# Kernel tuning notes

Hardware: AMD Instinct MI355X
Metric: run time of the kernel (lower is better)

## Reference

```python
import jax, jax.numpy as jnp
import numpy as np
from math import sqrt

LOCAL_WINDOW = 32
STRIDE = 64


def _sparse_mask(L):
    # L_Q == L_K path of DozerAttention:
    #  - local window: diagonals at offsets 0..local_window//2 (both signs)
    #  - strided: diagonals at offsets 0, stride+1, 2*(stride+1), ... (both signs)
    i = jnp.arange(L)[:, None]
    j = jnp.arange(L)[None, :]
    d = jnp.abs(i - j)
    local = d <= (LOCAL_WINDOW // 2)
    strided = (d % (STRIDE + 1)) == 0
    return (local | strided).astype(jnp.float32)  # [L, L]


def setup_inputs() -> dict:
    key = jax.random.key(0)
    B, L, H, D = 2, 2048, 8, 64
    kq, kk, kv = jax.random.split(key, 3)
    queries = jax.random.normal(kq, (B, L, H, D), dtype=jnp.float32)
    keys = jax.random.normal(kk, (B, L, H, D), dtype=jnp.float32)
    values = jax.random.normal(kv, (B, L, H, D), dtype=jnp.float32)
    # TriangularCausalMask: True above the diagonal -> masked with -inf
    causal = jnp.triu(jnp.ones((L, L), dtype=bool), k=1)
    attn_mask = jnp.broadcast_to(causal[None, None], (B, 1, L, L))
    return {"queries": queries, "keys": keys, "values": values, "attn_mask": attn_mask}


def reference(queries, keys, values, attn_mask):
    B, L, H, D = queries.shape
    scale = 1.0 / sqrt(D)
    sm = _sparse_mask(L)  # [L, L]
    # Original fills a zero-initialized dense score tensor only at selected key
    # columns per query row; equivalent to dense QK^T elementwise-masked by sm
    # (non-selected entries stay exactly 0, NOT -inf -- faithful quirk).
    scores = jnp.einsum('blhe,bshe->bhls', queries, keys) * sm  # [B,H,L,L]
    scores = jnp.where(attn_mask, -jnp.inf, scores)
    A = jax.nn.softmax(scale * scores, axis=-1)  # dropout p=0.0 in this config
    V = jnp.einsum('bhls,bshd->blhd', A, values)  # [B,L,H,D]
    return V
```

## Files before the change

kernel.cpp:

```cpp
#include <hip/hip_runtime.h>

#define B_ 2
#define L_ 2048
#define H_ 8
#define D_ 64
#define W_ 16
#define SP_ 65
#define NC_ 128
#define NL2_ 8

__global__ void chunk_sums_k(const float* __restrict__ v, float* __restrict__ csum1) {
    int blk = blockIdx.x;
    int c  = blk % NC_;
    int bh = blk / NC_;
    int h = bh % H_;
    int b = bh / H_;
    int d = threadIdx.x;
    float s = 0.f;
    int l0 = c * 16;
    #pragma unroll
    for (int l = 0; l < 16; ++l)
        s += v[((b * L_ + l0 + l) * H_ + h) * D_ + d];
    csum1[(bh * NC_ + c) * D_ + d] = s;
}

__global__ void l2_sums_k(const float* __restrict__ csum1, float* __restrict__ csum2) {
    int blk = blockIdx.x;
    int c2 = blk % NL2_;
    int bh = blk / NL2_;
    int d  = threadIdx.x;
    float s = 0.f;
    #pragma unroll
    for (int cc = 0; cc < 16; ++cc)
        s += csum1[(bh * NC_ + c2 * 16 + cc) * D_ + d];
    csum2[(bh * NL2_ + c2) * D_ + d] = s;
}

__global__ __launch_bounds__(256) void dozer_k(const float* __restrict__ q,
                                               const float* __restrict__ k,
                                               const float* __restrict__ v,
                                               const float* __restrict__ csum1,
                                               const float* __restrict__ csum2,
                                               float* __restrict__ out) {
    int gtid = blockIdx.x * blockDim.x + threadIdx.x;
    int wave = gtid >> 6;
    int lane = threadIdx.x & 63;
    int grp  = lane >> 3;
    int sub  = lane & 7;
    int i  = wave % L_;
    int hh = (wave / L_) % H_;
    int b  = wave / (L_ * H_);
    int bh = b * H_ + hh;

    const int rowstride = H_ * D_;
    const float* qp = q + ((size_t)(b * L_ + i) * H_ + hh) * D_ + 8 * sub;
    float4 qa = *(const float4*)qp;
    float4 qb = *(const float4*)(qp + 4);

    const float* kbase = k + ((size_t)b * L_ * H_ + hh) * D_ + 8 * sub;
    const float* vbase = v + ((size_t)b * L_ * H_ + hh) * D_ + 8 * sub;

    float4 na = make_float4(0.f, 0.f, 0.f, 0.f);
    float4 nb = make_float4(0.f, 0.f, 0.f, 0.f);
    float z = 0.f;

    int c1 = i >> 4;
    int c2 = i >> 8;
    int pstart = c1 << 4;

    int omax = (i < W_) ? i : W_;
    for (int o = grp; o <= omax; o += 8) {
        int j = i - o;
        const float* kr = kbase + (size_t)j * rowstride;
        const float* vr = vbase + (size_t)j * rowstride;
        float4 ka = *(const float4*)kr;
        float4 kb = *(const float4*)(kr + 4);
        float4 va = *(const float4*)vr;
        float4 vb = *(const float4*)(vr + 4);
        float part = qa.x * ka.x + qa.y * ka.y + qa.z * ka.z + qa.w * ka.w
                   + qb.x * kb.x + qb.y * kb.y + qb.z * kb.z + qb.w * kb.w;
        part += __shfl_xor(part, 1, 64);
        part += __shfl_xor(part, 2, 64);
        part += __shfl_xor(part, 4, 64);
        float we = __expf(0.125f * part) - 1.f;
        z += we;
        float wv = we + ((j >= pstart) ? 1.f : 0.f);
        na.x += wv * va.x; na.y += wv * va.y; na.z += wv * va.z; na.w += wv * va.w;
        nb.x += wv * vb.x; nb.y += wv * vb.y; nb.z += wv * vb.z; nb.w += wv * vb.w;
    }

    int tmax = i / SP_;
    for (int t = 1 + grp; t <= tmax; t += 8) {
        int j = i - SP_ * t;
        const float* kr = kbase + (size_t)j * rowstride;
        const float* vr = vbase + (size_t)j * rowstride;
        float4 ka = *(const float4*)kr;
        float4 kb = *(const float4*)(kr + 4);
        float4 va = *(const float4*)vr;
        float4 vb = *(const float4*)(vr + 4);
        float part = qa.x * ka.x + qa.y * ka.y + qa.z * ka.z + qa.w * ka.w
                   + qb.x * kb.x + qb.y * kb.y + qb.z * kb.z + qb.w * kb.w;
        part += __shfl_xor(part, 1, 64);
        part += __shfl_xor(part, 2, 64);
        part += __shfl_xor(part, 4, 64);
        float we = __expf(0.125f * part) - 1.f;
        z += we;
        na.x += we * va.x; na.y += we * va.y; na.z += we * va.z; na.w += we * va.w;
        nb.x += we * vb.x; nb.y += we * vb.y; nb.z += we * vb.z; nb.w += we * vb.w;
    }

    const float* cs2 = csum2 + ((size_t)bh * NL2_) * D_ + 8 * sub;
    for (int cc = grp; cc < c2; cc += 8) {
        float4 a = *(const float4*)(cs2 + (size_t)cc * D_);
        float4 bb = *(const float4*)(cs2 + (size_t)cc * D_ + 4);
        na.x += a.x; na.y += a.y; na.z += a.z; na.w += a.w;
        nb.x += bb.x; nb.y += bb.y; nb.z += bb.z; nb.w += bb.w;
    }
    const float* cs1 = csum1 + ((size_t)bh * NC_) * D_ + 8 * sub;
    for (int cc = (c2 << 4) + grp; cc < c1; cc += 8) {
        float4 a = *(const float4*)(cs1 + (size_t)cc * D_);
        float4 bb = *(const float4*)(cs1 + (size_t)cc * D_ + 4);
        na.x += a.x; na.y += a.y; na.z += a.z; na.w += a.w;
        nb.x += bb.x; nb.y += bb.y; nb.z += bb.z; nb.w += bb.w;
    }

    #pragma unroll
    for (int m = 8; m <= 32; m <<= 1) {
        na.x += __shfl_xor(na.x, m, 64); na.y += __shfl_xor(na.y, m, 64);
        na.z += __shfl_xor(na.z, m, 64); na.w += __shfl_xor(na.w, m, 64);
        nb.x += __shfl_xor(nb.x, m, 64); nb.y += __shfl_xor(nb.y, m, 64);
        nb.z += __shfl_xor(nb.z, m, 64); nb.w += __shfl_xor(nb.w, m, 64);
        z    += __shfl_xor(z, m, 64);
    }

    if (lane < 8) {
        float inv = 1.f / (z + (float)(i + 1));
        float* op = out + ((size_t)(b * L_ + i) * H_ + hh) * D_ + 8 * sub;
        float4 oa = make_float4(na.x * inv, na.y * inv, na.z * inv, na.w * inv);
        float4 ob = make_float4(nb.x * inv, nb.y * inv, nb.z * inv, nb.w * inv);
        *(float4*)op = oa;
        *(float4*)(op + 4) = ob;
    }
}

extern "C" void kernel_launch(void* const* d_in, const int* in_sizes, int n_in,
                              void* d_out, int out_size, void* d_ws, size_t ws_size,
                              hipStream_t stream) {
    const float* q = (const float*)d_in[0];
    const float* k = (const float*)d_in[1];
    const float* v = (const float*)d_in[2];
    float* out = (float*)d_out;

    float* csum1 = (float*)d_ws;
    float* csum2 = csum1 + (size_t)B_ * H_ * NC_ * D_;

    chunk_sums_k<<<B_ * H_ * NC_, 64, 0, stream>>>(v, csum1);
    l2_sums_k   <<<B_ * H_ * NL2_, 64, 0, stream>>>(csum1, csum2);

    int rows = B_ * H_ * L_;
    dozer_k<<<rows / 4, 256, 0, stream>>>(q, k, v, csum1, csum2, out);
}
```

Measured before the change: 124.5 us.

## Process two adjacent query rows per wave to share local-window K/V loads

Each wave now handles a pair of adjacent query rows (ia, ib). The local window loads 18 keys once and uses them for both rows, with predicates selecting which offsets count for each. The prefix chunk sums are also computed once and added to both rows, while the strided keys are still loaded separately per row. This halves the wave count and removes some redundant K/V and chunk-sum traffic, at the cost of more registers per thread and extra predication.

New measurement: 123.1 us. Within noise of the previous version (-1.1%).

```diff
diff --git a/kernel.cpp b/kernel.cpp
--- a/kernel.cpp
+++ b/kernel.cpp
@@ -47,99 +47,141 @@
     int lane = threadIdx.x & 63;
     int grp  = lane >> 3;
     int sub  = lane & 7;
-    int i  = wave % L_;
-    int hh = (wave / L_) % H_;
-    int b  = wave / (L_ * H_);
+    int pr = wave % (L_ / 2);
+    int hh = (wave / (L_ / 2)) % H_;
+    int b  = wave / ((L_ / 2) * H_);
     int bh = b * H_ + hh;
-
-    const int rowstride = H_ * D_;
-    const float* qp = q + ((size_t)(b * L_ + i) * H_ + hh) * D_ + 8 * sub;
-    float4 qa = *(const float4*)qp;
-    float4 qb = *(const float4*)(qp + 4);
+    int ia = 2 * pr;
+    int ib = ia + 1;
+
+    const int rs = H_ * D_;
+    const float* qpa = q + ((size_t)(b * L_ + ia) * H_ + hh) * D_ + 8 * sub;
+    float4 qa0 = *(const float4*)qpa;
+    float4 qa1 = *(const float4*)(qpa + 4);
+    float4 qb0 = *(const float4*)(qpa + rs);
+    float4 qb1 = *(const float4*)(qpa + rs + 4);
 
     const float* kbase = k + ((size_t)b * L_ * H_ + hh) * D_ + 8 * sub;
     const float* vbase = v + ((size_t)b * L_ * H_ + hh) * D_ + 8 * sub;
 
-    float4 na = make_float4(0.f, 0.f, 0.f, 0.f);
-    float4 nb = make_float4(0.f, 0.f, 0.f, 0.f);
-    float z = 0.f;
-
-    int c1 = i >> 4;
-    int c2 = i >> 8;
+    float4 na0 = make_float4(0.f,0.f,0.f,0.f), na1 = na0;
+    float4 nb0 = na0, nb1 = na0;
+    float za = 0.f, zb = 0.f;
+
+    int c1 = ia >> 4;
+    int c2 = ia >> 8;
     int pstart = c1 << 4;
 
-    int omax = (i < W_) ? i : W_;
-    for (int o = grp; o <= omax; o += 8) {
-        int j = i - o;
-        const float* kr = kbase + (size_t)j * rowstride;
-        const float* vr = vbase + (size_t)j * rowstride;
-        float4 ka = *(const float4*)kr;
-        float4 kb = *(const float4*)(kr + 4);
-        float4 va = *(const float4*)vr;
-        float4 vb = *(const float4*)(vr + 4);
-        float part = qa.x * ka.x + qa.y * ka.y + qa.z * ka.z + qa.w * ka.w
-                   + qb.x * kb.x + qb.y * kb.y + qb.z * kb.z + qb.w * kb.w;
-        part += __shfl_xor(part, 1, 64);
-        part += __shfl_xor(part, 2, 64);
-        part += __shfl_xor(part, 4, 64);
-        float we = __expf(0.125f * part) - 1.f;
-        z += we;
-        float wv = we + ((j >= pstart) ? 1.f : 0.f);
-        na.x += wv * va.x; na.y += wv * va.y; na.z += wv * va.z; na.w += wv * va.w;
-        nb.x += wv * vb.x; nb.y += wv * vb.y; nb.z += wv * vb.z; nb.w += wv * vb.w;
-    }
-
-    int tmax = i / SP_;
+    #pragma unroll
+    for (int it = 0; it < 3; ++it) {
+        int o = grp + 8 * it;
+        int j = ib - o;
+        bool jok = (o <= 17) && (j >= 0);
+        int jc = jok ? j : 0;
+        const float* kr = kbase + (size_t)jc * rs;
+        const float* vr = vbase + (size_t)jc * rs;
+        float4 k0 = *(const float4*)kr;
+        float4 k1 = *(const float4*)(kr + 4);
+        float4 v0 = *(const float4*)vr;
+        float4 v1 = *(const float4*)(vr + 4);
+        float pa = qa0.x*k0.x + qa0.y*k0.y + qa0.z*k0.z + qa0.w*k0.w
+                 + qa1.x*k1.x + qa1.y*k1.y + qa1.z*k1.z + qa1.w*k1.w;
+        float pb = qb0.x*k0.x + qb0.y*k0.y + qb0.z*k0.z + qb0.w*k0.w
+                 + qb1.x*k1.x + qb1.y*k1.y + qb1.z*k1.z + qb1.w*k1.w;
+        pa += __shfl_xor(pa, 1, 64); pb += __shfl_xor(pb, 1, 64);
+        pa += __shfl_xor(pa, 2, 64); pb += __shfl_xor(pb, 2, 64);
+        pa += __shfl_xor(pa, 4, 64); pb += __shfl_xor(pb, 4, 64);
+        bool act_a = jok && (o >= 1);
+        bool act_b = jok && (o <= 16);
+        float wa = act_a ? (__expf(0.125f * pa) - 1.f) : 0.f;
+        float wb = act_b ? (__expf(0.125f * pb) - 1.f) : 0.f;
+        za += wa; zb += wb;
+        float fa = wa + ((jok && o >= 1 && j >= pstart) ? 1.f : 0.f);
+        float fb = wb + ((jok && j >= pstart) ? 1.f : 0.f);
+        na0.x += fa*v0.x; na0.y += fa*v0.y; na0.z += fa*v0.z; na0.w += fa*v0.w;
+        na1.x += fa*v1.x; na1.y += fa*v1.y; na1.z += fa*v1.z; na1.w += fa*v1.w;
+        nb0.x += fb*v0.x; nb0.y += fb*v0.y; nb0.z += fb*v0.z; nb0.w += fb*v0.w;
+        nb1.x += fb*v1.x; nb1.y += fb*v1.y; nb1.z += fb*v1.z; nb1.w += fb*v1.w;
+    }
+
+    int tmax = ib / SP_;
     for (int t = 1 + grp; t <= tmax; t += 8) {
-        int j = i - SP_ * t;
-        const float* kr = kbase + (size_t)j * rowstride;
-        const float* vr = vbase + (size_t)j * rowstride;
-        float4 ka = *(const float4*)kr;
-        float4 kb = *(const float4*)(kr + 4);
-        float4 va = *(const float4*)vr;
-        float4 vb = *(const float4*)(vr + 4);
-        float part = qa.x * ka.x + qa.y * ka.y + qa.z * ka.z + qa.w * ka.w
-                   + qb.x * kb.x + qb.y * kb.y + qb.z * kb.z + qb.w * kb.w;
-        part += __shfl_xor(part, 1, 64);
-        part += __shfl_xor(part, 2, 64);
-        part += __shfl_xor(part, 4, 64);
-        float we = __expf(0.125f * part) - 1.f;
-        z += we;
-        na.x += we * va.x; na.y += we * va.y; na.z += we * va.z; na.w += we * va.w;
-        nb.x += we * vb.x; nb.y += we * vb.y; nb.z += we * vb.z; nb.w += we * vb.w;
-    }
-
-    const float* cs2 = csum2 + ((size_t)bh * NL2_) * D_ + 8 * sub;
+        int jb = ib - SP_ * t;
+        int ja = jb - 1;
+        bool aok = (ja >= 0);
+        int jac = aok ? ja : 0;
+        const float* kra = kbase + (size_t)jac * rs;
+        const float* vra = vbase + (size_t)jac * rs;
+        const float* krb = kbase + (size_t)jb * rs;
+        const float* vrb = vbase + (size_t)jb * rs;
+        float4 ka0 = *(const float4*)kra;
+        float4 ka1 = *(const float4*)(kra + 4);
+        float4 kb0 = *(const float4*)krb;
+        float4 kb1 = *(const float4*)(krb + 4);
+        float4 va0 = *(const float4*)vra;
+        float4 va1 = *(const float4*)(vra + 4);
+        float4 vb0 = *(const float4*)vrb;
+        float4 vb1 = *(const float4*)(vrb + 4);
+        float pa = qa0.x*ka0.x + qa0.y*ka0.y + qa0.z*ka0.z + qa0.w*ka0.w
+                 + qa1.x*ka1.x + qa1.y*ka1.y + qa1.z*ka1.z + qa1.w*ka1.w;
+        float pb = qb0.x*kb0.x + qb0.y*kb0.y + qb0.z*kb0.z + qb0.w*kb0.w
+                 + qb1.x*kb1.x + qb1.y*kb1.y + qb1.z*kb1.z + qb1.w*kb1.w;
+        pa += __shfl_xor(pa, 1, 64); pb += __shfl_xor(pb, 1, 64);
+        pa += __shfl_xor(pa, 2, 64); pb += __shfl_xor(pb, 2, 64);
+        pa += __shfl_xor(pa, 4, 64); pb += __shfl_xor(pb, 4, 64);
+        float wa = aok ? (__expf(0.125f * pa) - 1.f) : 0.f;
+        float wb = __expf(0.125f * pb) - 1.f;
+        za += wa; zb += wb;
+        na0.x += wa*va0.x; na0.y += wa*va0.y; na0.z += wa*va0.z; na0.w += wa*va0.w;
+        na1.x += wa*va1.x; na1.y += wa*va1.y; na1.z += wa*va1.z; na1.w += wa*va1.w;
+        nb0.x += wb*vb0.x; nb0.y += wb*vb0.y; nb0.z += wb*vb0.z; nb0.w += wb*vb0.w;
+        nb1.x += wb*vb1.x; nb1.y += wb*vb1.y; nb1.z += wb*vb1.z; nb1.w += wb*vb1.w;
+    }
+
+    float4 p0 = make_float4(0.f,0.f,0.f,0.f), p1 = p0;
+    const float* cs2 = csum2 + (size_t)bh * NL2_ * D_ + 8 * sub;
     for (int cc = grp; cc < c2; cc += 8) {
         float4 a = *(const float4*)(cs2 + (size_t)cc * D_);
-        float4 bb = *(const float4*)(cs2 + (size_t)cc * D_ + 4);
-        na.x += a.x; na.y += a.y; na.z += a.z; na.w += a.w;
-        nb.x += bb.x; nb.y += bb.y; nb.z += bb.z; nb.w += bb.w;
-    }
-    const float* cs1 = csum1 + ((size_t)bh * NC_) * D_ + 8 * sub;
+        float4 bq = *(const float4*)(cs2 + (size_t)cc * D_ + 4);
+        p0.x += a.x;  p0.y += a.y;  p0.z += a.z;  p0.w += a.w;
+        p1.x += bq.x; p1.y += bq.y; p1.z += bq.z; p1.w += bq.w;
+    }
+    const float* cs1 = csum1 + (size_t)bh * NC_ * D_ + 8 * sub;
     for (int cc = (c2 << 4) + grp; cc < c1; cc += 8) {
         float4 a = *(const float4*)(cs1 + (size_t)cc * D_);
-        float4 bb = *(const float4*)(cs1 + (size_t)cc * D_ + 4);
-        na.x += a.x; na.y += a.y; na.z += a.z; na.w += a.w;
-        nb.x += bb.x; nb.y += bb.y; nb.z += bb.z; nb.w += bb.w;
-    }
+        float4 bq = *(const float4*)(cs1 + (size_t)cc * D_ + 4);
+        p0.x += a.x;  p0.y += a.y;  p0.z += a.z;  p0.w += a.w;
+        p1.x += bq.x; p1.y += bq.y; p1.z += bq.z; p1.w += bq.w;
+    }
+    na0.x += p0.x; na0.y += p0.y; na0.z += p0.z; na0.w += p0.w;
+    na1.x += p1.x; na1.y += p1.y; na1.z += p1.z; na1.w += p1.w;
+    nb0.x += p0.x; nb0.y += p0.y; nb0.z += p0.z; nb0.w += p0.w;
+    nb1.x += p1.x; nb1.y += p1.y; nb1.z += p1.z; nb1.w += p1.w;
 
     #pragma unroll
     for (int m = 8; m <= 32; m <<= 1) {
-        na.x += __shfl_xor(na.x, m, 64); na.y += __shfl_xor(na.y, m, 64);
-        na.z += __shfl_xor(na.z, m, 64); na.w += __shfl_xor(na.w, m, 64);
-        nb.x += __shfl_xor(nb.x, m, 64); nb.y += __shfl_xor(nb.y, m, 64);
-        nb.z += __shfl_xor(nb.z, m, 64); nb.w += __shfl_xor(nb.w, m, 64);
-        z    += __shfl_xor(z, m, 64);
-    }
-
-    if (lane < 8) {
-        float inv = 1.f / (z + (float)(i + 1));
-        float* op = out + ((size_t)(b * L_ + i) * H_ + hh) * D_ + 8 * sub;
-        float4 oa = make_float4(na.x * inv, na.y * inv, na.z * inv, na.w * inv);
-        float4 ob = make_float4(nb.x * inv, nb.y * inv, nb.z * inv, nb.w * inv);
-        *(float4*)op = oa;
-        *(float4*)(op + 4) = ob;
+        na0.x += __shfl_xor(na0.x, m, 64); na0.y += __shfl_xor(na0.y, m, 64);
+        na0.z += __shfl_xor(na0.z, m, 64); na0.w += __shfl_xor(na0.w, m, 64);
+        na1.x += __shfl_xor(na1.x, m, 64); na1.y += __shfl_xor(na1.y, m, 64);
+        na1.z += __shfl_xor(na1.z, m, 64); na1.w += __shfl_xor(na1.w, m, 64);
+        nb0.x += __shfl_xor(nb0.x, m, 64); nb0.y += __shfl_xor(nb0.y, m, 64);
+        nb0.z += __shfl_xor(nb0.z, m, 64); nb0.w += __shfl_xor(nb0.w, m, 64);
+        nb1.x += __shfl_xor(nb1.x, m, 64); nb1.y += __shfl_xor(nb1.y, m, 64);
+        nb1.z += __shfl_xor(nb1.z, m, 64); nb1.w += __shfl_xor(nb1.w, m, 64);
+        za    += __shfl_xor(za, m, 64);
+        zb    += __shfl_xor(zb, m, 64);
+    }
+
+    if (grp == 0) {
+        float inv = 1.f / (za + (float)(ia + 1));
+        float* op = out + ((size_t)(b * L_ + ia) * H_ + hh) * D_ + 8 * sub;
+        *(float4*)op       = make_float4(na0.x*inv, na0.y*inv, na0.z*inv, na0.w*inv);
+        *(float4*)(op + 4) = make_float4(na1.x*inv, na1.y*inv, na1.z*inv, na1.w*inv);
+    } else if (grp == 1) {
+        float inv = 1.f / (zb + (float)(ib + 1));
+        float* op = out + ((size_t)(b * L_ + ib) * H_ + hh) * D_ + 8 * sub;
+        *(float4*)op       = make_float4(nb0.x*inv, nb0.y*inv, nb0.z*inv, nb0.w*inv);
+        *(float4*)(op + 4) = make_float4(nb1.x*inv, nb1.y*inv, nb1.z*inv, nb1.w*inv);
     }
 }
 
@@ -157,6 +199,6 @@
     chunk_sums_k<<<B_ * H_ * NC_, 64, 0, stream>>>(v, csum1);
     l2_sums_k   <<<B_ * H_ * NL2_, 64, 0, stream>>>(csum1, csum2);
 
-    int rows = B_ * H_ * L_;
-    dozer_k<<<rows / 4, 256, 0, stream>>>(q, k, v, csum1, csum2, out);
-}
+    int pairs = B_ * H_ * (L_ / 2);
+    dozer_k<<<pairs / 4, 256, 0, stream>>>(q, k, v, csum1, csum2, out);
+}
```

## Split each query row across two waves and combine partial sums in LDS

Applied to the files above, without the earlier changes.

Each query row is now handled by two waves, 16 key slots per row instead of 8, with the partial numerators and normalizers combined through shared memory after a block barrier. The grid doubles to compensate. The aim is to shorten the per-wave serial loop over the local, strided and prefix-sum terms, which cuts per-row latency and gives more parallelism. In exchange it adds a __syncthreads and LDS traffic, and duplicates the q load and setup work across both waves.

New measurement: 130.8 us. +5.1%, slower.

```diff
diff --git a/kernel.cpp b/kernel.cpp
--- a/kernel.cpp
+++ b/kernel.cpp
@@ -42,26 +42,31 @@
                                                const float* __restrict__ csum1,
                                                const float* __restrict__ csum2,
                                                float* __restrict__ out) {
-    int gtid = blockIdx.x * blockDim.x + threadIdx.x;
-    int wave = gtid >> 6;
+    __shared__ float sm[4][72];
+    __shared__ float zs[4];
+
     int lane = threadIdx.x & 63;
+    int wib  = threadIdx.x >> 6;
     int grp  = lane >> 3;
     int sub  = lane & 7;
-    int i  = wave % L_;
-    int hh = (wave / L_) % H_;
-    int b  = wave / (L_ * H_);
-    int bh = b * H_ + hh;
+    int half = wib & 1;
+    int slot = grp + 8 * half;
 
-    const int rowstride = H_ * D_;
+    int R  = 2 * blockIdx.x + (wib >> 1);
+    int i  = R & (L_ - 1);
+    int bh = R >> 11;
+    int hh = bh & (H_ - 1);
+    int b  = bh >> 3;
+
+    const int rs = H_ * D_;
     const float* qp = q + ((size_t)(b * L_ + i) * H_ + hh) * D_ + 8 * sub;
-    float4 qa = *(const float4*)qp;
-    float4 qb = *(const float4*)(qp + 4);
+    float4 q0 = *(const float4*)qp;
+    float4 q1 = *(const float4*)(qp + 4);
 
     const float* kbase = k + ((size_t)b * L_ * H_ + hh) * D_ + 8 * sub;
     const float* vbase = v + ((size_t)b * L_ * H_ + hh) * D_ + 8 * sub;
 
-    float4 na = make_float4(0.f, 0.f, 0.f, 0.f);
-    float4 nb = make_float4(0.f, 0.f, 0.f, 0.f);
+    float4 n0 = make_float4(0.f, 0.f, 0.f, 0.f), n1 = n0;
     float z = 0.f;
 
     int c1 = i >> 4;
@@ -69,77 +74,81 @@
     int pstart = c1 << 4;
 
     int omax = (i < W_) ? i : W_;
-    for (int o = grp; o <= omax; o += 8) {
+    for (int o = slot; o <= omax; o += 16) {
         int j = i - o;
-        const float* kr = kbase + (size_t)j * rowstride;
-        const float* vr = vbase + (size_t)j * rowstride;
-        float4 ka = *(const float4*)kr;
-        float4 kb = *(const float4*)(kr + 4);
-        float4 va = *(const float4*)vr;
-        float4 vb = *(const float4*)(vr + 4);
-        float part = qa.x * ka.x + qa.y * ka.y + qa.z * ka.z + qa.w * ka.w
-                   + qb.x * kb.x + qb.y * kb.y + qb.z * kb.z + qb.w * kb.w;
-        part += __shfl_xor(part, 1, 64);
-        part += __shfl_xor(part, 2, 64);
-        part += __shfl_xor(part, 4, 64);
-        float we = __expf(0.125f * part) - 1.f;
+        const float* kr = kbase + (size_t)j * rs;
+        const float* vr = vbase + (size_t)j * rs;
+        float4 k0 = *(const float4*)kr;
+        float4 k1 = *(const float4*)(kr + 4);
+        float4 v0 = *(const float4*)vr;
+        float4 v1 = *(const float4*)(vr + 4);
+        float p = q0.x*k0.x + q0.y*k0.y + q0.z*k0.z + q0.w*k0.w
+                + q1.x*k1.x + q1.y*k1.y + q1.z*k1.z + q1.w*k1.w;
+        p += __shfl_xor(p, 1, 64);
+        p += __shfl_xor(p, 2, 64);
+        p += __shfl_xor(p, 4, 64);
+        float we = __expf(0.125f * p) - 1.f;
         z += we;
         float wv = we + ((j >= pstart) ? 1.f : 0.f);
-        na.x += wv * va.x; na.y += wv * va.y; na.z += wv * va.z; na.w += wv * va.w;
-        nb.x += wv * vb.x; nb.y += wv * vb.y; nb.z += wv * vb.z; nb.w += wv * vb.w;
+        n0.x += wv*v0.x; n0.y += wv*v0.y; n0.z += wv*v0.z; n0.w += wv*v0.w;
+        n1.x += wv*v1.x; n1.y += wv*v1.y; n1.z += wv*v1.z; n1.w += wv*v1.w;
     }
 
     int tmax = i / SP_;
-    for (int t = 1 + grp; t <= tmax; t += 8) {
+    for (int t = 1 + slot; t <= tmax; t += 16) {
         int j = i - SP_ * t;
-        const float* kr = kbase + (size_t)j * rowstride;
-        const float* vr = vbase + (size_t)j * rowstride;
-        float4 ka = *(const float4*)kr;
-        float4 kb = *(const float4*)(kr + 4);
-        float4 va = *(const float4*)vr;
-        float4 vb = *(const float4*)(vr + 4);
-        float part = qa.x * ka.x + qa.y * ka.y + qa.z * ka.z + qa.w * ka.w
-                   + qb.x * kb.x + qb.y * kb.y + qb.z * kb.z + qb.w * kb.w;
-        part += __shfl_xor(part, 1, 64);
-        part += __shfl_xor(part, 2, 64);
-        part += __shfl_xor(part, 4, 64);
-        float we = __expf(0.125f * part) - 1.f;
+        const float* kr = kbase + (size_t)j * rs;
+        const float* vr = vbase + (size_t)j * rs;
+        float4 k0 = *(const float4*)kr;
+        float4 k1 = *(const float4*)(kr + 4);
+        float4 v0 = *(const float4*)vr;
+        float4 v1 = *(const float4*)(vr + 4);
+        float p = q0.x*k0.x + q0.y*k0.y + q0.z*k0.z + q0.w*k0.w
+                + q1.x*k1.x + q1.y*k1.y + q1.z*k1.z + q1.w*k1.w;
+        p += __shfl_xor(p, 1, 64);
+        p += __shfl_xor(p, 2, 64);
+        p += __shfl_xor(p, 4, 64);
+        float we = __expf(0.125f * p) - 1.f;
         z += we;
-        na.x += we * va.x; na.y += we * va.y; na.z += we * va.z; na.w += we * va.w;
-        nb.x += we * vb.x; nb.y += we * vb.y; nb.z += we * vb.z; nb.w += we * vb.w;
+        n0.x += we*v0.x; n0.y += we*v0.y; n0.z += we*v0.z; n0.w += we*v0.w;
+        n1.x += we*v1.x; n1.y += we*v1.y; n1.z += we*v1.z; n1.w += we*v1.w;
     }
 
-    const float* cs2 = csum2 + ((size_t)bh * NL2_) * D_ + 8 * sub;
-    for (int cc = grp; cc < c2; cc += 8) {
+    const float* cs2 = csum2 + (size_t)bh * NL2_ * D_ + 8 * sub;
+    for (int cc = slot; cc < c2; cc += 16) {
         float4 a = *(const float4*)(cs2 + (size_t)cc * D_);
         float4 bb = *(const float4*)(cs2 + (size_t)cc * D_ + 4);
-        na.x += a.x; na.y += a.y; na.z += a.z; na.w += a.w;
-        nb.x += bb.x; nb.y += bb.y; nb.z += bb.z; nb.w += bb.w;
+        n0.x += a.x;  n0.y += a.y;  n0.z += a.z;  n0.w += a.w;
+        n1.x += bb.x; n1.y += bb.y; n1.z += bb.z; n1.w += bb.w;
     }
-    const float* cs1 = csum1 + ((size_t)bh * NC_) * D_ + 8 * sub;
-    for (int cc = (c2 << 4) + grp; cc < c1; cc += 8) {
+    const float* cs1 = csum1 + (size_t)bh * NC_ * D_ + 8 * sub;
+    for (int cc = (c2 << 4) + slot; cc < c1; cc += 16) {
         float4 a = *(const float4*)(cs1 + (size_t)cc * D_);
         float4 bb = *(const float4*)(cs1 + (size_t)cc * D_ + 4);
-        na.x += a.x; na.y += a.y; na.z += a.z; na.w += a.w;
-        nb.x += bb.x; nb.y += bb.y; nb.z += bb.z; nb.w += bb.w;
+        n0.x += a.x;  n0.y += a.y;  n0.z += a.z;  n0.w += a.w;
+        n1.x += bb.x; n1.y += bb.y; n1.z += bb.z; n1.w += bb.w;
     }
 
     #pragma unroll
     for (int m = 8; m <= 32; m <<= 1) {
-        na.x += __shfl_xor(na.x, m, 64); na.y += __shfl_xor(na.y, m, 64);
-        na.z += __shfl_xor(na.z, m, 64); na.w += __shfl_xor(na.w, m, 64);
-        nb.x += __shfl_xor(nb.x, m, 64); nb.y += __shfl_xor(nb.y, m, 64);
-        nb.z += __shfl_xor(nb.z, m, 64); nb.w += __shfl_xor(nb.w, m, 64);
+        n0.x += __shfl_xor(n0.x, m, 64); n0.y += __shfl_xor(n0.y, m, 64);
+        n0.z += __shfl_xor(n0.z, m, 64); n0.w += __shfl_xor(n0.w, m, 64);
+        n1.x += __shfl_xor(n1.x, m, 64); n1.y += __shfl_xor(n1.y, m, 64);
+        n1.z += __shfl_xor(n1.z, m, 64); n1.w += __shfl_xor(n1.w, m, 64);
         z    += __shfl_xor(z, m, 64);
     }
 
-    if (lane < 8) {
-        float inv = 1.f / (z + (float)(i + 1));
-        float* op = out + ((size_t)(b * L_ + i) * H_ + hh) * D_ + 8 * sub;
-        float4 oa = make_float4(na.x * inv, na.y * inv, na.z * inv, na.w * inv);
-        float4 ob = make_float4(nb.x * inv, nb.y * inv, nb.z * inv, nb.w * inv);
-        *(float4*)op = oa;
-        *(float4*)(op + 4) = ob;
+    if (grp == 0) {
+        *(float4*)&sm[wib][sub * 8]     = n0;
+        *(float4*)&sm[wib][sub * 8 + 4] = n1;
+        if (sub == 0) zs[wib] = z;
+    }
+    __syncthreads();
+
+    if (half == 0) {
+        float val = sm[wib][lane] + sm[wib + 1][lane];
+        float inv = 1.f / (zs[wib] + zs[wib + 1] + (float)(i + 1));
+        out[((size_t)(b * L_ + i) * H_ + hh) * D_ + lane] = val * inv;
     }
 }
 
@@ -157,6 +166,6 @@
     chunk_sums_k<<<B_ * H_ * NC_, 64, 0, stream>>>(v, csum1);
     l2_sums_k   <<<B_ * H_ * NL2_, 64, 0, stream>>>(csum1, csum2);
 
-    int rows = B_ * H_ * L_;
-    dozer_k<<<rows / 4, 256, 0, stream>>>(q, k, v, csum1, csum2, out);
+    int blocks = B_ * H_ * L_ / 2;
+    dozer_k<<<blocks, 256, 0, stream>>>(q, k, v, csum1, csum2, out);
 }
```
